# Optimization experiments

Hardware: AMD Instinct MI355X
Metric: run time of the kernel (lower is better)

Reference implementation:

```python
import jax, jax.numpy as jnp
import numpy as np

B, N, D, H = 4096, 64, 32, 64

def setup_inputs() -> dict:
    key = jax.random.key(0)
    ks = jax.random.split(key, 10)
    s = lambda fan_in: 1.0 / np.sqrt(fan_in)
    return {
        "joint_features": jax.random.normal(ks[0], (B, N, D), jnp.float32),
        "Wm1": jax.random.uniform(ks[1], (2 * D, H), jnp.float32, -s(2 * D), s(2 * D)),
        "bm1": jax.random.uniform(ks[2], (H,), jnp.float32, -s(2 * D), s(2 * D)),
        "Wm2": jax.random.uniform(ks[3], (H, D), jnp.float32, -s(H), s(H)),
        "bm2": jax.random.uniform(ks[4], (D,), jnp.float32, -s(H), s(H)),
        "Wu1": jax.random.uniform(ks[5], (2 * D, H), jnp.float32, -s(2 * D), s(2 * D)),
        "bu1": jax.random.uniform(ks[6], (H,), jnp.float32, -s(2 * D), s(2 * D)),
        "Wu2": jax.random.uniform(ks[7], (H, D), jnp.float32, -s(H), s(H)),
        "bu2": jax.random.uniform(ks[8], (D,), jnp.float32, -s(H), s(H)),
        "residual_weight": jnp.float32(0.5),
        "num_joints": N,
    }

def reference(joint_features, Wm1, bm1, Wm2, bm2, Wu1, bu1, Wu2, bu2, residual_weight, num_joints):
    n = num_joints
    # chain topology: directed edges (i->i+1) and (i+1->i); dst receives message
    dst = jnp.concatenate([jnp.arange(n - 1), jnp.arange(1, n)])  # [E]
    src = jnp.concatenate([jnp.arange(1, n), jnp.arange(n - 1)])  # [E]
    # edge gather + concat: [B, E, 2D]
    edge_in = jnp.concatenate([joint_features[:, dst], joint_features[:, src]], axis=-1)
    # message MLP (ReLU after both layers, per original Sequential)
    msg = jax.nn.relu(jax.nn.relu(edge_in @ Wm1 + bm1) @ Wm2 + bm2)  # [B, E, D]
    # scatter-add messages to destination nodes
    messages = jnp.zeros_like(joint_features).at[:, dst].add(msg)  # [B, N, D]
    # per-node update MLP on concat(feature, message)
    upd_in = jnp.concatenate([joint_features, messages], axis=-1)  # [B, N, 2D]
    updated = jax.nn.relu(upd_in @ Wu1 + bu1) @ Wu2 + bu2  # [B, N, D]
    return residual_weight * updated + (1.0 - residual_weight) * joint_features
```

## Files before the change

kernel.cpp:

```cpp
#include <hip/hip_runtime.h>
#include <hip/hip_bf16.h>


typedef __bf16 bf16x8 __attribute__((ext_vector_type(8)));
typedef float  f32x4  __attribute__((ext_vector_type(4)));
typedef unsigned short u16;

#define HS  72
#define MBS 40

__device__ __forceinline__ u16 f2b(float f) { return __builtin_bit_cast(u16, (__bf16)f); }
__device__ __forceinline__ f32x4 MFMA(bf16x8 a, bf16x8 b, f32x4 c) {
    return __builtin_amdgcn_mfma_f32_16x16x32_bf16(a, b, c, 0, 0, 0);
}
__device__ __forceinline__ bf16x8 pack8(float4 a, float4 b) {
    bf16x8 r = {(__bf16)a.x, (__bf16)a.y, (__bf16)a.z, (__bf16)a.w,
                (__bf16)b.x, (__bf16)b.y, (__bf16)b.z, (__bf16)b.w};
    return r;
}

__global__ void agn_prep(const float* __restrict__ Wm1, const float* __restrict__ bm1,
                         const float* __restrict__ Wm2, const float* __restrict__ bm2,
                         const float* __restrict__ Wu1, const float* __restrict__ bu1,
                         const float* __restrict__ Wu2, const float* __restrict__ bu2,
                         const float* __restrict__ rw,
                         u16* __restrict__ wsf, float* __restrict__ wsb)
{
    const int idx = blockIdx.x * 256 + threadIdx.x;
    {
        const int f = idx >> 9, r = idx & 511;
        const int lane = r >> 3, j = r & 7;
        const int ln = lane & 15, q = lane >> 4;
        float v;
        if (f < 4)       v = Wm1[(q * 8 + j) * 64 + f * 16 + ln];
        else if (f < 8)  v = Wm1[(32 + q * 8 + j) * 64 + (f - 4) * 16 + ln];
        else if (f < 12) { int s = (f - 8) >> 1, nt = (f - 8) & 1;  v = Wm2[(s * 32 + q * 8 + j) * 32 + nt * 16 + ln]; }
        else if (f < 20) { int s = (f - 12) >> 2, nt = (f - 12) & 3; v = Wu1[(s * 32 + q * 8 + j) * 64 + nt * 16 + ln]; }
        else             { int s = (f - 20) >> 1, nt = (f - 20) & 1; v = Wu2[(s * 32 + q * 8 + j) * 32 + nt * 16 + ln]; }
        wsf[idx] = f2b(v);
    }
    if (blockIdx.x == 0) {
        const int t = threadIdx.x;
        if (t < 192) {
            const int g = t >> 4, i = t & 15;
            float v;
            if (g < 4)       v = bm1[g * 16 + i];
            else if (g < 6)  v = bm2[(g - 4) * 16 + i];
            else if (g < 10) v = bu1[(g - 6) * 16 + i];
            else             v = bu2[(g - 10) * 16 + i];
            wsb[t] = v;
        }
        if (t == 255) wsb[192] = rw[0];
    }
}

__global__ __launch_bounds__(256, 4)
void agn_main(const float* __restrict__ x, const u16* __restrict__ wsf,
              const float* __restrict__ wsb, float* __restrict__ out)
{
    __shared__ __align__(16) u16 sH[128 * HS];
    __shared__ __align__(16) u16 sMB[128 * MBS];

    const int t = threadIdx.x;
    const int w = t >> 6;
    const int lane = t & 63;
    const int ln = lane & 15;
    const int q  = lane >> 4;

    const size_t base = (size_t)blockIdx.x * (64 * 32);
    const float* xb = x + base;
    float*       ob = out + base;

    const u16* wf = wsf + lane * 8;
#define LDFRAG(f) __builtin_bit_cast(bf16x8, *(const uint4*)(wf + ((f) << 9)))

    {
        bf16x8 B1a[4], B1b[4];
#pragma unroll
        for (int nt = 0; nt < 4; ++nt) { B1a[nt] = LDFRAG(nt); B1b[nt] = LDFRAG(4 + nt); }
        float bm1v[4];
#pragma unroll
        for (int nt = 0; nt < 4; ++nt) bm1v[nt] = wsb[nt * 16 + ln];
#pragma unroll
        for (int m = 0; m < 2; ++m) {
            const int mt = 2 * w + m;
            int e = mt * 16 + ln;
            if (e >= 126) e = 0;
            const int dst  = (e < 63) ? e : e - 62;
            const int srcn = (e < 63) ? e + 1 : e - 63;
            const float* pd = xb + dst * 32 + q * 8;
            const float* ps = xb + srcn * 32 + q * 8;
            float4 d0 = *(const float4*)pd, d1 = *(const float4*)(pd + 4);
            float4 s0 = *(const float4*)ps, s1 = *(const float4*)(ps + 4);
            bf16x8 Ad = pack8(d0, d1);
            bf16x8 As = pack8(s0, s1);
#pragma unroll
            for (int nt = 0; nt < 4; ++nt) {
                f32x4 acc = {0.f, 0.f, 0.f, 0.f};
                acc = MFMA(Ad, B1a[nt], acc);
                acc = MFMA(As, B1b[nt], acc);
                const int rb = mt * 16 + q * 4;
                const int c  = nt * 16 + ln;
#pragma unroll
                for (int r = 0; r < 4; ++r)
                    sH[(rb + r) * HS + c] = f2b(fmaxf(acc[r] + bm1v[nt], 0.f));
            }
        }
    }
    __syncthreads();

    {
        bf16x8 B2[2][2];
#pragma unroll
        for (int s = 0; s < 2; ++s)
#pragma unroll
            for (int nt = 0; nt < 2; ++nt) B2[s][nt] = LDFRAG(8 + s * 2 + nt);
        float bm2v[2] = { wsb[64 + ln], wsb[80 + ln] };
#pragma unroll
        for (int m = 0; m < 2; ++m) {
            const int mt = 2 * w + m;
            const int row = mt * 16 + ln;
            bf16x8 A0 = __builtin_bit_cast(bf16x8, *(const uint4*)&sH[row * HS + q * 8]);
            bf16x8 A1 = __builtin_bit_cast(bf16x8, *(const uint4*)&sH[row * HS + 32 + q * 8]);
#pragma unroll
            for (int nt = 0; nt < 2; ++nt) {
                f32x4 acc = {0.f, 0.f, 0.f, 0.f};
                acc = MFMA(A0, B2[0][nt], acc);
                acc = MFMA(A1, B2[1][nt], acc);
                const int rb = mt * 16 + q * 4;
                const int c  = nt * 16 + ln;
#pragma unroll
                for (int r = 0; r < 4; ++r)
                    sMB[(rb + r) * MBS + c] = f2b(fmaxf(acc[r] + bm2v[nt], 0.f));
            }
        }
    }
    __syncthreads();

    {
        bf16x8 B3[2][4];
#pragma unroll
        for (int s = 0; s < 2; ++s)
#pragma unroll
            for (int nt = 0; nt < 4; ++nt) B3[s][nt] = LDFRAG(12 + s * 4 + nt);
        float bu1v[4];
#pragma unroll
        for (int nt = 0; nt < 4; ++nt) bu1v[nt] = wsb[96 + nt * 16 + ln];
        const int row = w * 16 + ln;
        const float* p = xb + row * 32 + q * 8;
        float4 a0 = *(const float4*)p, a1 = *(const float4*)(p + 4);
        bf16x8 A0 = pack8(a0, a1);
        float mv[8] = {0.f, 0.f, 0.f, 0.f, 0.f, 0.f, 0.f, 0.f};
        if (row < 63) {
            uint4 u = *(const uint4*)&sMB[row * MBS + q * 8];
            const unsigned* pu = (const unsigned*)&u;
#pragma unroll
            for (int h = 0; h < 4; ++h) {
                mv[2 * h]     += __uint_as_float(pu[h] << 16);
                mv[2 * h + 1] += __uint_as_float(pu[h] & 0xFFFF0000u);
            }
        }
        if (row > 0) {
            uint4 u = *(const uint4*)&sMB[(62 + row) * MBS + q * 8];
            const unsigned* pu = (const unsigned*)&u;
#pragma unroll
            for (int h = 0; h < 4; ++h) {
                mv[2 * h]     += __uint_as_float(pu[h] << 16);
                mv[2 * h + 1] += __uint_as_float(pu[h] & 0xFFFF0000u);
            }
        }
        bf16x8 A1;
#pragma unroll
        for (int j = 0; j < 8; ++j) A1[j] = (__bf16)mv[j];
#pragma unroll
        for (int nt = 0; nt < 4; ++nt) {
            f32x4 acc = {0.f, 0.f, 0.f, 0.f};
            acc = MFMA(A0, B3[0][nt], acc);
            acc = MFMA(A1, B3[1][nt], acc);
            const int rb = w * 16 + q * 4;
            const int c  = nt * 16 + ln;
#pragma unroll
            for (int r = 0; r < 4; ++r)
                sH[(rb + r) * HS + c] = f2b(fmaxf(acc[r] + bu1v[nt], 0.f));
        }
    }
    __syncthreads();

    {
        bf16x8 B4[2][2];
#pragma unroll
        for (int s = 0; s < 2; ++s)
#pragma unroll
            for (int nt = 0; nt < 2; ++nt) B4[s][nt] = LDFRAG(20 + s * 2 + nt);
        float bu2v[2] = { wsb[160 + ln], wsb[176 + ln] };
        const float rw = wsb[192];
        const float om = 1.f - rw;
        const int arow = w * 16 + ln;
        bf16x8 A0 = __builtin_bit_cast(bf16x8, *(const uint4*)&sH[arow * HS + q * 8]);
        bf16x8 A1 = __builtin_bit_cast(bf16x8, *(const uint4*)&sH[arow * HS + 32 + q * 8]);
#pragma unroll
        for (int nt = 0; nt < 2; ++nt) {
            f32x4 acc = {0.f, 0.f, 0.f, 0.f};
            acc = MFMA(A0, B4[0][nt], acc);
            acc = MFMA(A1, B4[1][nt], acc);
            const int rb = w * 16 + q * 4;
            const int c  = nt * 16 + ln;
#pragma unroll
            for (int r = 0; r < 4; ++r) {
                const int off = (rb + r) * 32 + c;
                ob[off] = rw * (acc[r] + bu2v[nt]) + om * xb[off];
            }
        }
    }
#undef LDFRAG
}

extern "C" void kernel_launch(void* const* d_in, const int* in_sizes, int n_in,
                              void* d_out, int out_size, void* d_ws, size_t ws_size,
                              hipStream_t stream) {
    const float* x   = (const float*)d_in[0];
    const float* Wm1 = (const float*)d_in[1];
    const float* bm1 = (const float*)d_in[2];
    const float* Wm2 = (const float*)d_in[3];
    const float* bm2 = (const float*)d_in[4];
    const float* Wu1 = (const float*)d_in[5];
    const float* bu1 = (const float*)d_in[6];
    const float* Wu2 = (const float*)d_in[7];
    const float* bu2 = (const float*)d_in[8];
    const float* rw  = (const float*)d_in[9];
    float* out = (float*)d_out;

    u16*   wsf = (u16*)d_ws;
    float* wsb = (float*)((char*)d_ws + 24576);

    const int B = in_sizes[0] / (64 * 32);
    agn_prep<<<48, 256, 0, stream>>>(Wm1, bm1, Wm2, bm2, Wu1, bu1, Wu2, bu2, rw, wsf, wsb);
    agn_main<<<B, 256, 0, stream>>>(x, wsf, wsb, out);
}
```

Measured before the change: 127.2 us.

## Give each wavefront its own batch element and drop block-wide barriers

Each wavefront now processes a full batch element independently, using per-wave LDS patches and message buffers, so all __syncthreads barriers go away and the grid shrinks to B/4 blocks. Layer 1 and layer 2 of each MLP are fused per 16-row tile through a small LDS patch. Biases are folded into the accumulator initial value. It adds register pressure, since more weight fragments stay live, and lowers the launch bound to 3 blocks per CU. The larger per-wave LDS footprint may also limit occupancy, and the grid has fewer blocks.

```diff
diff --git a/kernel.cpp b/kernel.cpp
--- a/kernel.cpp
+++ b/kernel.cpp
@@ -6,7 +6,7 @@
 typedef float  f32x4  __attribute__((ext_vector_type(4)));
 typedef unsigned short u16;
 
-#define HS  72
+#define PS  72
 #define MBS 40
 
 __device__ __forceinline__ u16 f2b(float f) { return __builtin_bit_cast(u16, (__bf16)f); }
@@ -54,12 +54,12 @@
     }
 }
 
-__global__ __launch_bounds__(256, 4)
+__global__ __launch_bounds__(256, 3)
 void agn_main(const float* __restrict__ x, const u16* __restrict__ wsf,
               const float* __restrict__ wsb, float* __restrict__ out)
 {
-    __shared__ __align__(16) u16 sH[128 * HS];
-    __shared__ __align__(16) u16 sMB[128 * MBS];
+    __shared__ __align__(16) u16 sPatch[4][16 * PS];
+    __shared__ __align__(16) u16 sMB[4][128 * MBS];
 
     const int t = threadIdx.x;
     const int w = t >> 6;
@@ -67,7 +67,10 @@
     const int ln = lane & 15;
     const int q  = lane >> 4;
 
-    const size_t base = (size_t)blockIdx.x * (64 * 32);
+    u16* patch = sPatch[w];
+    u16* mb    = sMB[w];
+
+    const size_t base = ((size_t)blockIdx.x * 4 + w) * (64 * 32);
     const float* xb = x + base;
     float*       ob = out + base;
 
@@ -75,16 +78,21 @@
 #define LDFRAG(f) __builtin_bit_cast(bf16x8, *(const uint4*)(wf + ((f) << 9)))
 
     {
-        bf16x8 B1a[4], B1b[4];
+        bf16x8 B1a[4], B1b[4], B2[2][2];
 #pragma unroll
         for (int nt = 0; nt < 4; ++nt) { B1a[nt] = LDFRAG(nt); B1b[nt] = LDFRAG(4 + nt); }
+#pragma unroll
+        for (int s = 0; s < 2; ++s)
+#pragma unroll
+            for (int nt = 0; nt < 2; ++nt) B2[s][nt] = LDFRAG(8 + s * 2 + nt);
         float bm1v[4];
 #pragma unroll
         for (int nt = 0; nt < 4; ++nt) bm1v[nt] = wsb[nt * 16 + ln];
-#pragma unroll
-        for (int m = 0; m < 2; ++m) {
-            const int mt = 2 * w + m;
-            int e = mt * 16 + ln;
+        float bm2v[2] = { wsb[64 + ln], wsb[80 + ln] };
+
+#pragma unroll 2
+        for (int et = 0; et < 8; ++et) {
+            int e = et * 16 + ln;
             if (e >= 126) e = 0;
             const int dst  = (e < 63) ? e : e - 62;
             const int srcn = (e < 63) ? e + 1 : e - 63;
@@ -96,119 +104,97 @@
             bf16x8 As = pack8(s0, s1);
 #pragma unroll
             for (int nt = 0; nt < 4; ++nt) {
-                f32x4 acc = {0.f, 0.f, 0.f, 0.f};
+                f32x4 acc = {bm1v[nt], bm1v[nt], bm1v[nt], bm1v[nt]};
                 acc = MFMA(Ad, B1a[nt], acc);
                 acc = MFMA(As, B1b[nt], acc);
-                const int rb = mt * 16 + q * 4;
-                const int c  = nt * 16 + ln;
+                const int c = nt * 16 + ln;
 #pragma unroll
                 for (int r = 0; r < 4; ++r)
-                    sH[(rb + r) * HS + c] = f2b(fmaxf(acc[r] + bm1v[nt], 0.f));
-            }
-        }
-    }
-    __syncthreads();
-
-    {
-        bf16x8 B2[2][2];
-#pragma unroll
-        for (int s = 0; s < 2; ++s)
-#pragma unroll
-            for (int nt = 0; nt < 2; ++nt) B2[s][nt] = LDFRAG(8 + s * 2 + nt);
-        float bm2v[2] = { wsb[64 + ln], wsb[80 + ln] };
-#pragma unroll
-        for (int m = 0; m < 2; ++m) {
-            const int mt = 2 * w + m;
-            const int row = mt * 16 + ln;
-            bf16x8 A0 = __builtin_bit_cast(bf16x8, *(const uint4*)&sH[row * HS + q * 8]);
-            bf16x8 A1 = __builtin_bit_cast(bf16x8, *(const uint4*)&sH[row * HS + 32 + q * 8]);
+                    patch[(q * 4 + r) * PS + c] = f2b(fmaxf(acc[r], 0.f));
+            }
+            bf16x8 A0 = __builtin_bit_cast(bf16x8, *(const uint4*)&patch[ln * PS + q * 8]);
+            bf16x8 A1 = __builtin_bit_cast(bf16x8, *(const uint4*)&patch[ln * PS + 32 + q * 8]);
 #pragma unroll
             for (int nt = 0; nt < 2; ++nt) {
-                f32x4 acc = {0.f, 0.f, 0.f, 0.f};
+                f32x4 acc = {bm2v[nt], bm2v[nt], bm2v[nt], bm2v[nt]};
                 acc = MFMA(A0, B2[0][nt], acc);
                 acc = MFMA(A1, B2[1][nt], acc);
-                const int rb = mt * 16 + q * 4;
-                const int c  = nt * 16 + ln;
+                const int c = nt * 16 + ln;
 #pragma unroll
                 for (int r = 0; r < 4; ++r)
-                    sMB[(rb + r) * MBS + c] = f2b(fmaxf(acc[r] + bm2v[nt], 0.f));
+                    mb[(et * 16 + q * 4 + r) * MBS + c] = f2b(fmaxf(acc[r], 0.f));
             }
         }
     }
-    __syncthreads();
 
     {
-        bf16x8 B3[2][4];
+        bf16x8 B3[2][4], B4[2][2];
 #pragma unroll
         for (int s = 0; s < 2; ++s)
 #pragma unroll
             for (int nt = 0; nt < 4; ++nt) B3[s][nt] = LDFRAG(12 + s * 4 + nt);
+#pragma unroll
+        for (int s = 0; s < 2; ++s)
+#pragma unroll
+            for (int nt = 0; nt < 2; ++nt) B4[s][nt] = LDFRAG(20 + s * 2 + nt);
         float bu1v[4];
 #pragma unroll
         for (int nt = 0; nt < 4; ++nt) bu1v[nt] = wsb[96 + nt * 16 + ln];
-        const int row = w * 16 + ln;
-        const float* p = xb + row * 32 + q * 8;
-        float4 a0 = *(const float4*)p, a1 = *(const float4*)(p + 4);
-        bf16x8 A0 = pack8(a0, a1);
-        float mv[8] = {0.f, 0.f, 0.f, 0.f, 0.f, 0.f, 0.f, 0.f};
-        if (row < 63) {
-            uint4 u = *(const uint4*)&sMB[row * MBS + q * 8];
-            const unsigned* pu = (const unsigned*)&u;
-#pragma unroll
-            for (int h = 0; h < 4; ++h) {
-                mv[2 * h]     += __uint_as_float(pu[h] << 16);
-                mv[2 * h + 1] += __uint_as_float(pu[h] & 0xFFFF0000u);
-            }
-        }
-        if (row > 0) {
-            uint4 u = *(const uint4*)&sMB[(62 + row) * MBS + q * 8];
-            const unsigned* pu = (const unsigned*)&u;
-#pragma unroll
-            for (int h = 0; h < 4; ++h) {
-                mv[2 * h]     += __uint_as_float(pu[h] << 16);
-                mv[2 * h + 1] += __uint_as_float(pu[h] & 0xFFFF0000u);
-            }
-        }
-        bf16x8 A1;
-#pragma unroll
-        for (int j = 0; j < 8; ++j) A1[j] = (__bf16)mv[j];
-#pragma unroll
-        for (int nt = 0; nt < 4; ++nt) {
-            f32x4 acc = {0.f, 0.f, 0.f, 0.f};
-            acc = MFMA(A0, B3[0][nt], acc);
-            acc = MFMA(A1, B3[1][nt], acc);
-            const int rb = w * 16 + q * 4;
-            const int c  = nt * 16 + ln;
-#pragma unroll
-            for (int r = 0; r < 4; ++r)
-                sH[(rb + r) * HS + c] = f2b(fmaxf(acc[r] + bu1v[nt], 0.f));
-        }
-    }
-    __syncthreads();
-
-    {
-        bf16x8 B4[2][2];
-#pragma unroll
-        for (int s = 0; s < 2; ++s)
-#pragma unroll
-            for (int nt = 0; nt < 2; ++nt) B4[s][nt] = LDFRAG(20 + s * 2 + nt);
         float bu2v[2] = { wsb[160 + ln], wsb[176 + ln] };
-        const float rw = wsb[192];
-        const float om = 1.f - rw;
-        const int arow = w * 16 + ln;
-        bf16x8 A0 = __builtin_bit_cast(bf16x8, *(const uint4*)&sH[arow * HS + q * 8]);
-        bf16x8 A1 = __builtin_bit_cast(bf16x8, *(const uint4*)&sH[arow * HS + 32 + q * 8]);
-#pragma unroll
-        for (int nt = 0; nt < 2; ++nt) {
-            f32x4 acc = {0.f, 0.f, 0.f, 0.f};
-            acc = MFMA(A0, B4[0][nt], acc);
-            acc = MFMA(A1, B4[1][nt], acc);
-            const int rb = w * 16 + q * 4;
-            const int c  = nt * 16 + ln;
-#pragma unroll
-            for (int r = 0; r < 4; ++r) {
-                const int off = (rb + r) * 32 + c;
-                ob[off] = rw * (acc[r] + bu2v[nt]) + om * xb[off];
+        const float rwv = wsb[192];
+        const float om  = 1.f - rwv;
+
+#pragma unroll 2
+        for (int nt4 = 0; nt4 < 4; ++nt4) {
+            const int row = nt4 * 16 + ln;
+            const float* p = xb + row * 32 + q * 8;
+            float4 a0 = *(const float4*)p, a1 = *(const float4*)(p + 4);
+            bf16x8 A0 = pack8(a0, a1);
+            float mv[8] = {0.f, 0.f, 0.f, 0.f, 0.f, 0.f, 0.f, 0.f};
+            if (row < 63) {
+                uint4 u = *(const uint4*)&mb[row * MBS + q * 8];
+                const unsigned* pu = (const unsigned*)&u;
+#pragma unroll
+                for (int h = 0; h < 4; ++h) {
+                    mv[2 * h]     += __uint_as_float(pu[h] << 16);
+                    mv[2 * h + 1] += __uint_as_float(pu[h] & 0xFFFF0000u);
+                }
+            }
+            if (row > 0) {
+                uint4 u = *(const uint4*)&mb[(62 + row) * MBS + q * 8];
+                const unsigned* pu = (const unsigned*)&u;
+#pragma unroll
+                for (int h = 0; h < 4; ++h) {
+                    mv[2 * h]     += __uint_as_float(pu[h] << 16);
+                    mv[2 * h + 1] += __uint_as_float(pu[h] & 0xFFFF0000u);
+                }
+            }
+            bf16x8 A1;
+#pragma unroll
+            for (int j = 0; j < 8; ++j) A1[j] = (__bf16)mv[j];
+#pragma unroll
+            for (int nt = 0; nt < 4; ++nt) {
+                f32x4 acc = {bu1v[nt], bu1v[nt], bu1v[nt], bu1v[nt]};
+                acc = MFMA(A0, B3[0][nt], acc);
+                acc = MFMA(A1, B3[1][nt], acc);
+                const int c = nt * 16 + ln;
+#pragma unroll
+                for (int r = 0; r < 4; ++r)
+                    patch[(q * 4 + r) * PS + c] = f2b(fmaxf(acc[r], 0.f));
+            }
+            bf16x8 H0 = __builtin_bit_cast(bf16x8, *(const uint4*)&patch[ln * PS + q * 8]);
+            bf16x8 H1 = __builtin_bit_cast(bf16x8, *(const uint4*)&patch[ln * PS + 32 + q * 8]);
+#pragma unroll
+            for (int nt = 0; nt < 2; ++nt) {
+                f32x4 acc = {bu2v[nt], bu2v[nt], bu2v[nt], bu2v[nt]};
+                acc = MFMA(H0, B4[0][nt], acc);
+                acc = MFMA(H1, B4[1][nt], acc);
+                const int c = nt * 16 + ln;
+#pragma unroll
+                for (int r = 0; r < 4; ++r) {
+                    const int off = (nt4 * 16 + q * 4 + r) * 32 + c;
+                    ob[off] = rwv * acc[r] + om * xb[off];
+                }
             }
         }
     }
@@ -235,5 +221,5 @@
 
     const int B = in_sizes[0] / (64 * 32);
     agn_prep<<<48, 256, 0, stream>>>(Wm1, bm1, Wm2, bm2, Wu1, bu1, Wu2, bu2, rw, wsf, wsb);
-    agn_main<<<B, 256, 0, stream>>>(x, wsf, wsb, out);
-}
+    agn_main<<<B / 4, 256, 0, stream>>>(x, wsf, wsb, out);
+}
```

Result: faster. 124.1 us (-2.5%).
